# Kernel tuning notes

Hardware: AMD Instinct MI355X
Metric: run time of the kernel (lower is better)

Reference implementation:

```python
import jax, jax.numpy as jnp
import numpy as np

DEPTH, DIM, HEADS, DHEAD, MLP, CTX_DIM = 4, 1024, 16, 64, 4096, 1024
INNER = HEADS * DHEAD
SCALE = DHEAD ** -0.5
B, N, M = 4, 1024, 2048


def setup_inputs() -> dict:
    key = jax.random.key(0)
    ks = jax.random.split(key, 16)
    w = lambda k, shape: jax.random.normal(k, shape, dtype=jnp.float32) * 0.02
    return {
        "x": jax.random.normal(ks[0], (B, N, DIM), dtype=jnp.float32),
        "context": jax.random.normal(ks[1], (B, M, CTX_DIM), dtype=jnp.float32),
        "mask": jnp.ones((B, N), dtype=jnp.int32),
        # LayerNorm params: index 0 = pre-self-attn, 1 = pre-cross-attn, 2 = pre-FFN
        "ln_g": jnp.ones((DEPTH, 3, DIM), dtype=jnp.float32),
        "ln_b": jnp.zeros((DEPTH, 3, DIM), dtype=jnp.float32),
        "Wqkv": w(ks[2], (DEPTH, DIM, 3 * INNER)),
        "Wo_sa": w(ks[3], (DEPTH, INNER, DIM)),
        "bo_sa": jnp.zeros((DEPTH, DIM), dtype=jnp.float32),
        "Wkv": w(ks[4], (DEPTH, CTX_DIM, 2 * INNER)),
        "Wq": w(ks[5], (DEPTH, DIM, INNER)),
        "Wo_ca": w(ks[6], (DEPTH, INNER, DIM)),
        "bo_ca": jnp.zeros((DEPTH, DIM), dtype=jnp.float32),
        "W1": w(ks[7], (DEPTH, DIM, MLP)),
        "b1": jnp.zeros((DEPTH, MLP), dtype=jnp.float32),
        "W2": w(ks[8], (DEPTH, MLP, DIM)),
        "b2": jnp.zeros((DEPTH, DIM), dtype=jnp.float32),
    }


def _ln(x, g, b, eps=1e-5):
    mu = jnp.mean(x, axis=-1, keepdims=True)
    var = jnp.var(x, axis=-1, keepdims=True)
    return (x - mu) * jax.lax.rsqrt(var + eps) * g + b


def _split_heads(t):  # [b, n, h*d] -> [b, h, n, d]
    b, n, _ = t.shape
    return t.reshape(b, n, HEADS, DHEAD).transpose(0, 2, 1, 3)


def _merge_heads(t):  # [b, h, n, d] -> [b, n, h*d]
    b, h, n, d = t.shape
    return t.transpose(0, 2, 1, 3).reshape(b, n, h * d)


def _forward(x, context, mask, ln_g, ln_b, Wqkv, Wo_sa, bo_sa, Wkv, Wq, Wo_ca, bo_ca, W1, b1, W2, b2):
    neg_mask = (1 - mask).astype(x.dtype)  # [b, n]
    for i in range(DEPTH):
        # ---- self-attention (PreNorm) ----
        h = _ln(x, ln_g[i, 0], ln_b[i, 0])
        qkv = h @ Wqkv[i]
        q, k, v = jnp.split(qkv, 3, axis=-1)
        q, k, v = _split_heads(q), _split_heads(k), _split_heads(v)
        dots = jnp.einsum('bhnd,bhmd->bhnm', q, k) * SCALE
        dots = dots - neg_mask[:, None, None, :] * 1e11  # mask over keys
        attn = jax.nn.softmax(dots, axis=-1)
        out = _merge_heads(jnp.einsum('bhnm,bhmd->bhnd', attn, v))
        x = x + out @ Wo_sa[i] + bo_sa[i]
        # ---- cross-attention (PreNorm) ----
        h = _ln(x, ln_g[i, 1], ln_b[i, 1])
        kv = context @ Wkv[i]
        k, v = jnp.split(kv, 2, axis=-1)
        q = _split_heads(h @ Wq[i])
        k, v = _split_heads(k), _split_heads(v)
        dots = jnp.einsum('bhnd,bhmd->bhnm', q, k) * SCALE  # [b, h, n, m]
        dots = dots - neg_mask[:, None, :, None] * 1e6  # mask over queries
        attn = jax.nn.softmax(dots, axis=-1)
        out = _merge_heads(jnp.einsum('bhnm,bhmd->bhnd', attn, v))
        x = x + out @ Wo_ca[i] + bo_ca[i]
        # ---- feed-forward (PreNorm) ----
        h = _ln(x, ln_g[i, 2], ln_b[i, 2])
        h = jax.nn.gelu(h @ W1[i] + b1[i], approximate=False)
        x = x + h @ W2[i] + b2[i]
    return x


def reference(x, context, mask, ln_g, ln_b, Wqkv, Wo_sa, bo_sa, Wkv, Wq, Wo_ca, bo_ca, W1, b1, W2, b2):
    return _forward(x, context, mask, ln_g, ln_b, Wqkv, Wo_sa, bo_sa, Wkv, Wq, Wo_ca, bo_ca, W1, b1, W2, b2)
```

## Files before the change

kernel.cpp:

```cpp
#include <hip/hip_runtime.h>
#include <math.h>

#define DEPTH_ 4
#define DIM_ 1024
#define HEADS_ 16
#define DHEAD_ 64
#define MLP_ 4096
#define CTX_ 1024
#define INNER_ 1024
#define B_ 4
#define N_ 1024
#define M_ 2048

typedef unsigned short u16;
typedef __attribute__((ext_vector_type(4))) unsigned short u16x4;
typedef __attribute__((ext_vector_type(8))) short bf16x8;
typedef __attribute__((ext_vector_type(4))) float f32x4;
typedef __attribute__((ext_vector_type(4))) int i32x4;

#define SCQ 0.18033688011112042f

__device__ __forceinline__ u16 f2bf(float f) {
    unsigned u = __float_as_uint(f);
    return (u16)((u + 0x7fffu + ((u >> 16) & 1u)) >> 16);
}

__device__ __forceinline__ float bf2f(u16 v) {
    return __uint_as_float(((unsigned)v) << 16);
}

__device__ __forceinline__ float exp2_fast(float x) {
    float r;
    asm("v_exp_f32 %0, %1" : "=v"(r) : "v"(x));
    return r;
}

__device__ __forceinline__ float rcp_fast(float x) {
    float r;
    asm("v_rcp_f32 %0, %1" : "=v"(r) : "v"(x));
    return r;
}

__device__ __forceinline__ unsigned cvt_pk_bf16(float lo, float hi) {
    unsigned r;
    asm("v_cvt_pk_bf16_f32 %0, %1, %2" : "=v"(r) : "v"(lo), "v"(hi));
    return r;
}

__device__ __forceinline__ float gelu_fast(float v) {
    float t = v + 0.044715f * v * v * v;
    float e = exp2_fast(-2.302221673f * t);
    return v * rcp_fast(1.0f + e);
}

#define GLOAD16(gp, sp)                                                        \
    __builtin_amdgcn_global_load_lds(                                          \
        (const __attribute__((address_space(1))) void*)(gp),                   \
        (__attribute__((address_space(3))) void*)(sp), 16, 0, 0)

template <int MODE>
__global__ __launch_bounds__(256) void ln_res(
    float* __restrict__ x, const u16* __restrict__ d0,
    const u16* __restrict__ d1, const float* __restrict__ dbias,
    const float* __restrict__ g, const float* __restrict__ b,
    u16* __restrict__ y) {
    int row = blockIdx.x;
    float4 v = ((const float4*)(x + (size_t)row * DIM_))[threadIdx.x];
    if constexpr (MODE == 1) {
        u16x4 a0 = ((const u16x4*)(d0 + (size_t)row * DIM_))[threadIdx.x];
        u16x4 a1 = ((const u16x4*)(d1 + (size_t)row * DIM_))[threadIdx.x];
        float4 bb4 = ((const float4*)dbias)[threadIdx.x];
        v.x += bf2f(a0[0]) + bf2f(a1[0]) + bb4.x;
        v.y += bf2f(a0[1]) + bf2f(a1[1]) + bb4.y;
        v.z += bf2f(a0[2]) + bf2f(a1[2]) + bb4.z;
        v.w += bf2f(a0[3]) + bf2f(a1[3]) + bb4.w;
        ((float4*)(x + (size_t)row * DIM_))[threadIdx.x] = v;
    }
    float s  = v.x + v.y + v.z + v.w;
    float ss = v.x * v.x + v.y * v.y + v.z * v.z + v.w * v.w;
    #pragma unroll
    for (int off = 32; off; off >>= 1) {
        s  += __shfl_down(s, off);
        ss += __shfl_down(ss, off);
    }
    __shared__ float red[10];
    int wid = threadIdx.x >> 6, lane = threadIdx.x & 63;
    if (lane == 0) { red[wid] = s; red[4 + wid] = ss; }
    __syncthreads();
    if (threadIdx.x == 0) {
        float ts  = red[0] + red[1] + red[2] + red[3];
        float tss = red[4] + red[5] + red[6] + red[7];
        float mu  = ts * (1.0f / DIM_);
        float var = tss * (1.0f / DIM_) - mu * mu;
        red[8] = mu;
        red[9] = rsqrtf(var + 1e-5f);
    }
    __syncthreads();
    float mu = red[8], rs = red[9];
    float4 gg = ((const float4*)g)[threadIdx.x];
    float4 bb = ((const float4*)b)[threadIdx.x];
    u16x4 o;
    o[0] = f2bf((v.x - mu) * rs * gg.x + bb.x);
    o[1] = f2bf((v.y - mu) * rs * gg.y + bb.y);
    o[2] = f2bf((v.z - mu) * rs * gg.z + bb.z);
    o[3] = f2bf((v.w - mu) * rs * gg.w + bb.w);
    ((u16x4*)(y + (size_t)row * DIM_))[threadIdx.x] = o;
}

__global__ __launch_bounds__(256) void res_add(
    float* __restrict__ x, const u16* __restrict__ d0,
    const u16* __restrict__ d1, const float* __restrict__ dbias) {
    int row = blockIdx.x;
    float4 v = ((const float4*)(x + (size_t)row * DIM_))[threadIdx.x];
    u16x4 a0 = ((const u16x4*)(d0 + (size_t)row * DIM_))[threadIdx.x];
    u16x4 a1 = ((const u16x4*)(d1 + (size_t)row * DIM_))[threadIdx.x];
    float4 bb4 = ((const float4*)dbias)[threadIdx.x];
    v.x += bf2f(a0[0]) + bf2f(a1[0]) + bb4.x;
    v.y += bf2f(a0[1]) + bf2f(a1[1]) + bb4.y;
    v.z += bf2f(a0[2]) + bf2f(a1[2]) + bb4.z;
    v.w += bf2f(a0[3]) + bf2f(a1[3]) + bb4.w;
    ((float4*)(x + (size_t)row * DIM_))[threadIdx.x] = v;
}

__global__ __launch_bounds__(256) void cast_kernel(const float* __restrict__ in,
                                                   u16* __restrict__ out) {
    int i = blockIdx.x * 256 + threadIdx.x;
    float4 v = ((const float4*)in)[i];
    u16x4 o = {f2bf(v.x), f2bf(v.y), f2bf(v.z), f2bf(v.w)};
    ((u16x4*)out)[i] = o;
}

struct PrepArgs {
    const float* src[7];
    int K[7];
    int N[7];
    int dstOff[7];
    int tileCum[7];
};

__global__ __launch_bounds__(256) void prep_weights(PrepArgs a,
                                                    u16* __restrict__ wt) {
    __shared__ float tile[32][33];
    int bid = blockIdx.x;
    int wi = 0;
    while (bid >= a.tileCum[wi]) ++wi;
    int tbase = wi ? a.tileCum[wi - 1] : 0;
    int tid = bid - tbase;
    int Kd = a.K[wi], Nd = a.N[wi];
    int ntx = Nd >> 5;
    int bx = (tid % ntx) * 32;
    int by = (tid / ntx) * 32;
    const float* W = a.src[wi];
    u16* Wt = wt + a.dstOff[wi];

    int t = threadIdx.x;
    int kl = t >> 3, n4 = (t & 7) * 4;
    float4 v = *(const float4*)(W + (size_t)(by + kl) * Nd + bx + n4);
    tile[kl][n4 + 0] = v.x; tile[kl][n4 + 1] = v.y;
    tile[kl][n4 + 2] = v.z; tile[kl][n4 + 3] = v.w;
    __syncthreads();
    int nl = t >> 3, k4 = (t & 7) * 4;
    u16x4 o;
    #pragma unroll
    for (int j = 0; j < 4; ++j) o[j] = f2bf(tile[k4 + j][nl]);
    *(u16x4*)(Wt + (size_t)(bx + nl) * Kd + by + k4) = o;
}

template <int EPI, int SPLITK>
__global__ __launch_bounds__(256, 3) void gemm_mfma3(
    const u16* __restrict__ A, const u16* __restrict__ Bt,
    const float* __restrict__ bias, void* __restrict__ Cout,
    u16* __restrict__ vt, int Mdim, int Ndim, int Kdim, int nx, int ny) {
    __shared__ __align__(16) u16 As[3][128 * 32];
    __shared__ __align__(16) u16 Bs[3][128 * 32];
    const int t = threadIdx.x;
    const int lane = t & 63, w = t >> 6;
    const int c = lane & 15, g = lane >> 4;
    const int wy = w >> 1, wx = w & 1;

    const int nwg = gridDim.x;
    const int wid = (blockIdx.x & 7) * (nwg >> 3) + (blockIdx.x >> 3);
    const int bx = wid % nx;
    const int by = (wid / nx) % ny;
    const int bz = wid / (nx * ny);
    const int m0 = by * 128, n0 = bx * 128;

    f32x4 acc[4][4] = {};

    const int srow = w * 32 + (lane >> 2);
    const int scb  = (((lane & 3) ^ ((srow >> 1) & 3)) * 8);
    const u16* Ag = A + (size_t)(m0 + srow) * Kdim + scb;
    const u16* Bg = Bt + (size_t)(n0 + srow) * Kdim + scb;

    auto stage = [&](int buf, int k0) {
        GLOAD16(Ag + k0, &As[buf][w * 1024]);
        GLOAD16(Ag + k0 + (size_t)16 * Kdim, &As[buf][w * 1024 + 512]);
        GLOAD16(Bg + k0, &Bs[buf][w * 1024]);
        GLOAD16(Bg + k0 + (size_t)16 * Kdim, &Bs[buf][w * 1024 + 512]);
    };
    const int rsw = (c >> 1) & 3;
    auto compute = [&](int buf) {
        bf16x8 a[4], b[4];
        #pragma unroll
        for (int i = 0; i < 4; ++i)
            a[i] = *(const bf16x8*)&As[buf][(wy * 64 + i * 16 + c) * 32 +
                                            ((g ^ rsw) * 8)];
        #pragma unroll
        for (int j = 0; j < 4; ++j)
            b[j] = *(const bf16x8*)&Bs[buf][(wx * 64 + j * 16 + c) * 32 +
                                            ((g ^ rsw) * 8)];
        __builtin_amdgcn_s_setprio(1);
        #pragma unroll
        for (int i = 0; i < 4; ++i)
            #pragma unroll
            for (int j = 0; j < 4; ++j)
                acc[i][j] = __builtin_amdgcn_mfma_f32_16x16x32_bf16(
                    a[i], b[j], acc[i][j], 0, 0, 0);
        __builtin_amdgcn_s_setprio(0);
    };

    const int kchunk = Kdim / SPLITK;
    const int kbeg = bz * kchunk;
    const int nsteps = kchunk / 32;

    stage(0, kbeg);
    stage(1, kbeg + 32);
    int cb = 0, sb = 2;
    for (int s = 0; s < nsteps; ++s) {
        if (s + 1 < nsteps)
            asm volatile("s_waitcnt vmcnt(4)" ::: "memory");
        else
            asm volatile("s_waitcnt vmcnt(0)" ::: "memory");
        __builtin_amdgcn_s_barrier();
        if (s + 2 < nsteps) {
            stage(sb, kbeg + (s + 2) * 32);
            sb = (sb == 2) ? 0 : sb + 1;
        }
        compute(cb);
        cb = (cb == 2) ? 0 : cb + 1;
    }

    constexpr int VTHRESH = (EPI == 4) ? 2048 : 1024;
    constexpr int RPB     = (EPI == 4) ? 1024 : 2048;
    constexpr int KVL     = (EPI == 4) ? 1024 : 2048;

    const size_t outOff = (SPLITK > 1) ? (size_t)bz * Mdim * Ndim : 0;

    #pragma unroll
    for (int i = 0; i < 4; ++i) {
        int row0 = m0 + wy * 64 + i * 16 + g * 4;
        #pragma unroll
        for (int j = 0; j < 4; ++j) {
            int col = n0 + wx * 64 + j * 16 + c;
            u16x4 o4;
            #pragma unroll
            for (int r = 0; r < 4; ++r) {
                float v = acc[i][j][r];
                size_t idx = (size_t)(row0 + r) * Ndim + col;
                if constexpr (EPI == 0) {
                    ((u16*)Cout)[outOff + idx] = f2bf(v);
                } else if constexpr (EPI == 4) {
                    if (col < 1024) v *= SCQ;
                    u16 bv = f2bf(v);
                    ((u16*)Cout)[idx] = bv;
                    o4[r] = bv;
                } else if constexpr (EPI == 5) {
                    u16 bv = f2bf(v);
                    ((u16*)Cout)[idx] = bv;
                    o4[r] = bv;
                } else if constexpr (EPI == 6) {
                    ((u16*)Cout)[idx] = f2bf(v * SCQ);
                } else if constexpr (EPI == 1) {
                    v += bias[col];
                    ((u16*)Cout)[idx] = f2bf(gelu_fast(v));
                }
            }
            if constexpr (EPI == 4 || EPI == 5) {
                if (n0 + wx * 64 + j * 16 >= VTHRESH) {
                    int hh = (col - VTHRESH) >> 6;
                    int dd = col & 63;
                    int bi = row0 / RPB;
                    int kv = row0 % RPB;
                    *(u16x4*)&vt[(((size_t)bi * HEADS_ + hh) * 64 + dd) * KVL +
                                 kv] = o4;
                }
            }
        }
    }
}

template <int KLEN, int IS_SA>
__global__ __launch_bounds__(256) void attn_mfma2(
    const u16* __restrict__ Qsrc, const u16* __restrict__ Ksrc,
    const u16* __restrict__ Vtg, const int* __restrict__ mask,
    u16* __restrict__ O) {
    constexpr int QSTR = IS_SA ? 3 * INNER_ : INNER_;
    constexpr int KSTR = IS_SA ? 3 * INNER_ : 2 * INNER_;
    constexpr int KOFF = IS_SA ? INNER_ : 0;

    __shared__ __align__(16) u16 Ks[2][64 * 64];
    __shared__ __align__(16) u16 Vs[2][64 * 64];

    const int t = threadIdx.x;
    const int lane = t & 63, w = t >> 6;
    const int c = lane & 15, g = lane >> 4;

    const int nwg = gridDim.x;
    const int wid = (blockIdx.x & 7) * (nwg >> 3) + (blockIdx.x >> 3);
    const int qb = wid & 15;
    const int h  = (wid >> 4) & 15;
    const int bb = wid >> 8;
    const int q0 = qb * 64;
    const int kvbase = bb * KLEN;

    const u16* qp =
        Qsrc + (size_t)(bb * N_ + q0 + w * 16 + c) * QSTR + h * 64 + g * 8;
    bf16x8 qf[2];
    qf[0] = *(const bf16x8*)qp;
    qf[1] = *(const bf16x8*)(qp + 32);

    const int sl_r = lane >> 3;
    const int scol = ((lane & 7) ^ sl_r) * 8;
    const int r0 = w * 16, r1 = w * 16 + 8;
    const u16* Kg0 = Ksrc + (size_t)(kvbase + r0 + sl_r) * KSTR + KOFF +
                     h * 64 + scol;
    const u16* Kg1 = Ksrc + (size_t)(kvbase + r1 + sl_r) * KSTR + KOFF +
                     h * 64 + scol;
    const u16* Vg0 =
        Vtg + ((size_t)(bb * HEADS_ + h) * 64 + r0 + sl_r) * KLEN + scol;
    const u16* Vg1 =
        Vtg + ((size_t)(bb * HEADS_ + h) * 64 + r1 + sl_r) * KLEN + scol;

    auto stageKV = [&](int buf, int kt) {
        GLOAD16(Kg0 + (size_t)kt * 64 * KSTR, &Ks[buf][r0 * 64]);
        GLOAD16(Kg1 + (size_t)kt * 64 * KSTR, &Ks[buf][r1 * 64]);
        GLOAD16(Vg0 + kt * 64, &Vs[buf][r0 * 64]);
        GLOAD16(Vg1 + kt * 64, &Vs[buf][r1 * 64]);
    };

    f32x4 o[4] = {};
    float mr = -1e30f, lr = 0.f;
    const int srcA = c + 32 * (g & 1);
    const int srcB = srcA + 16;
    const bool hi = (g & 2) != 0;
    constexpr int NT = KLEN / 64;

    stageKV(0, 0);
    __syncthreads();
    int cur = 0;

    for (int kt = 0; kt < NT; ++kt) {
        if (kt + 1 < NT) stageKV(cur ^ 1, kt + 1);

        f32x4 sv[4] = {};
        #pragma unroll
        for (int kvb = 0; kvb < 4; ++kvb) {
            #pragma unroll
            for (int f = 0; f < 2; ++f) {
                bf16x8 kf = *(const bf16x8*)&Ks[cur][(kvb * 16 + c) * 64 +
                                                     (((g + 4 * f) ^ (c & 7)) * 8)];
                sv[kvb] = __builtin_amdgcn_mfma_f32_16x16x32_bf16(
                    kf, qf[f], sv[kvb], 0, 0, 0);
            }
        }

        if constexpr (IS_SA) {
            int mbit = mask[bb * N_ + kt * 64 + lane];
            unsigned long long ball = __ballot(mbit != 0);
            if (ball != ~0ull) {
                float negm_reg = mbit ? 0.f : 2.0e10f;
                #pragma unroll
                for (int kvb = 0; kvb < 4; ++kvb)
                    #pragma unroll
                    for (int r = 0; r < 4; ++r)
                        sv[kvb][r] -= __shfl(negm_reg, kvb * 16 + g * 4 + r);
            }
        }

        float tm = sv[0][0];
        #pragma unroll
        for (int kvb = 0; kvb < 4; ++kvb)
            #pragma unroll
            for (int r = 0; r < 4; ++r) tm = fmaxf(tm, sv[kvb][r]);
        tm = fmaxf(tm, __shfl_xor(tm, 16));
        tm = fmaxf(tm, __shfl_xor(tm, 32));

        if (!__all(tm - mr <= 8.0f)) {
            float mn = fmaxf(mr, tm);
            float corr = exp2_fast(mr - mn);
            mr = mn;
            lr *= corr;
            float corrO[4];
            #pragma unroll
            for (int r = 0; r < 4; ++r) corrO[r] = __shfl(corr, g * 4 + r);
            #pragma unroll
            for (int db = 0; db < 4; ++db)
                #pragma unroll
                for (int r = 0; r < 4; ++r) o[db][r] *= corrO[r];
        }

        float ps = 0.f;
        #pragma unroll
        for (int kvb = 0; kvb < 4; ++kvb)
            #pragma unroll
            for (int r = 0; r < 4; ++r) {
                float p = exp2_fast(sv[kvb][r] - mr);
                sv[kvb][r] = p;
                ps += p;
            }
        ps += __shfl_xor(ps, 16);
        ps += __shfl_xor(ps, 32);
        lr += ps;

        unsigned pk[4][2];
        #pragma unroll
        for (int kvb = 0; kvb < 4; ++kvb)
            #pragma unroll
            for (int j = 0; j < 2; ++j)
                pk[kvb][j] = cvt_pk_bf16(sv[kvb][2 * j], sv[kvb][2 * j + 1]);

        #pragma unroll
        for (int pv = 0; pv < 2; ++pv) {
            int a0 = __shfl((int)pk[2 * pv][0], srcA);
            int b0 = __shfl((int)pk[2 * pv + 1][0], srcA);
            int a1 = __shfl((int)pk[2 * pv][1], srcA);
            int b1 = __shfl((int)pk[2 * pv + 1][1], srcA);
            int a2 = __shfl((int)pk[2 * pv][0], srcB);
            int b2 = __shfl((int)pk[2 * pv + 1][0], srcB);
            int a3 = __shfl((int)pk[2 * pv][1], srcB);
            int b3 = __shfl((int)pk[2 * pv + 1][1], srcB);
            i32x4 tw = {hi ? b0 : a0, hi ? b1 : a1, hi ? b2 : a2,
                        hi ? b3 : a3};
            bf16x8 pa = *(bf16x8*)&tw;
            #pragma unroll
            for (int db = 0; db < 4; ++db) {
                bf16x8 vf = *(const bf16x8*)&Vs[cur][(db * 16 + c) * 64 +
                                                     (((g + 4 * pv) ^ (c & 7)) * 8)];
                o[db] = __builtin_amdgcn_mfma_f32_16x16x32_bf16(pa, vf, o[db],
                                                                0, 0, 0);
            }
        }
        __syncthreads();
        cur ^= 1;
    }

    float inv = rcp_fast(lr);
    float invO[4];
    #pragma unroll
    for (int r = 0; r < 4; ++r) invO[r] = __shfl(inv, g * 4 + r);
    #pragma unroll
    for (int db = 0; db < 4; ++db)
        #pragma unroll
        for (int r = 0; r < 4; ++r) {
            size_t idx =
                (size_t)(bb * N_ + q0 + w * 16 + g * 4 + r) * INNER_ +
                h * 64 + db * 16 + c;
            O[idx] = f2bf(o[db][r] * invO[r]);
        }
}

extern "C" void kernel_launch(void* const* d_in, const int* in_sizes, int n_in,
                              void* d_out, int out_size, void* d_ws,
                              size_t ws_size, hipStream_t stream) {
    const float* x     = (const float*)d_in[0];
    const float* ctx   = (const float*)d_in[1];
    const int*   mask  = (const int*)d_in[2];
    const float* ln_g  = (const float*)d_in[3];
    const float* ln_b  = (const float*)d_in[4];
    const float* Wqkv  = (const float*)d_in[5];
    const float* Wo_sa = (const float*)d_in[6];
    const float* bo_sa = (const float*)d_in[7];
    const float* Wkv   = (const float*)d_in[8];
    const float* Wq    = (const float*)d_in[9];
    const float* Wo_ca = (const float*)d_in[10];
    const float* bo_ca = (const float*)d_in[11];
    const float* W1    = (const float*)d_in[12];
    const float* b1    = (const float*)d_in[13];
    const float* W2    = (const float*)d_in[14];
    const float* b2    = (const float*)d_in[15];
    float* xout = (float*)d_out;

    char* ws = (char*)d_ws;
    u16* lnout = (u16*)ws;
    u16* big   = (u16*)(ws + (8ull << 20));
    u16* qca   = (u16*)(ws + (40ull << 20));
    u16* ctxb  = (u16*)(ws + (48ull << 20));
    u16* wt    = (u16*)(ws + (64ull << 20));
    u16* vt_sa = (u16*)(ws + (96ull << 20));
    u16* R1    = (u16*)(ws + (104ull << 20));
    u16* aout  = lnout;

    const int O_QKV = 0;
    const int O_WOSA = 3145728;
    const int O_WQ   = 4194304;
    const int O_WKV  = 5242880;
    const int O_WOCA = 7340032;
    const int O_W1   = 8388608;
    const int O_W2   = 12582912;

    hipMemcpyAsync(xout, x, sizeof(float) * B_ * N_ * DIM_,
                   hipMemcpyDeviceToDevice, stream);
    cast_kernel<<<B_ * M_ * CTX_ / 1024, 256, 0, stream>>>(ctx, ctxb);

    const int ROWS = B_ * N_;
    const int CROWS = B_ * M_;
    const int HALF = ROWS * DIM_;
    dim3 blk(256);

    for (int i = 0; i < DEPTH_; ++i) {
        const float* g  = ln_g + (size_t)(i * 3) * DIM_;
        const float* bb = ln_b + (size_t)(i * 3) * DIM_;

        PrepArgs pa;
        pa.src[0] = Wqkv  + (size_t)i * DIM_ * 3 * INNER_;
        pa.src[1] = Wo_sa + (size_t)i * INNER_ * DIM_;
        pa.src[2] = Wq    + (size_t)i * DIM_ * INNER_;
        pa.src[3] = Wkv   + (size_t)i * CTX_ * 2 * INNER_;
        pa.src[4] = Wo_ca + (size_t)i * INNER_ * DIM_;
        pa.src[5] = W1    + (size_t)i * DIM_ * MLP_;
        pa.src[6] = W2    + (size_t)i * MLP_ * DIM_;
        int Ks_[7] = {1024, 1024, 1024, 1024, 1024, 1024, 4096};
        int Ns_[7] = {3072, 1024, 1024, 2048, 1024, 4096, 1024};
        int Of_[7] = {O_QKV, O_WOSA, O_WQ, O_WKV, O_WOCA, O_W1, O_W2};
        int cum = 0;
        for (int k = 0; k < 7; ++k) {
            pa.K[k] = Ks_[k]; pa.N[k] = Ns_[k]; pa.dstOff[k] = Of_[k];
            cum += (Ks_[k] / 32) * (Ns_[k] / 32);
            pa.tileCum[k] = cum;
        }
        prep_weights<<<cum, blk, 0, stream>>>(pa, wt);

        if (i == 0)
            ln_res<0><<<ROWS, blk, 0, stream>>>(xout, nullptr, nullptr,
                                                nullptr, g, bb, lnout);
        else
            ln_res<1><<<ROWS, blk, 0, stream>>>(xout, R1, R1 + HALF,
                                                b2 + (size_t)(i - 1) * DIM_,
                                                g, bb, lnout);
        gemm_mfma3<4, 1><<<24 * 32, blk, 0, stream>>>(
            lnout, wt + O_QKV, nullptr, big, vt_sa, ROWS, 3 * INNER_, DIM_,
            24, 32);
        attn_mfma2<N_, 1><<<1024, blk, 0, stream>>>(big, big, vt_sa, mask,
                                                    aout);
        gemm_mfma3<0, 2><<<8 * 32 * 2, blk, 0, stream>>>(
            aout, wt + O_WOSA, nullptr, R1, nullptr, ROWS, DIM_, INNER_,
            8, 32);

        ln_res<1><<<ROWS, blk, 0, stream>>>(xout, R1, R1 + HALF,
                                            bo_sa + (size_t)i * DIM_,
                                            g + DIM_, bb + DIM_, lnout);
        gemm_mfma3<6, 1><<<8 * 32, blk, 0, stream>>>(
            lnout, wt + O_WQ, nullptr, qca, nullptr, ROWS, INNER_, DIM_,
            8, 32);
        gemm_mfma3<5, 1><<<16 * 64, blk, 0, stream>>>(
            ctxb, wt + O_WKV, nullptr, big, R1, CROWS, 2 * INNER_, CTX_,
            16, 64);
        attn_mfma2<M_, 0><<<1024, blk, 0, stream>>>(qca, big, R1, mask,
                                                    aout);
        gemm_mfma3<0, 2><<<8 * 32 * 2, blk, 0, stream>>>(
            aout, wt + O_WOCA, nullptr, R1, nullptr, ROWS, DIM_, INNER_,
            8, 32);

        ln_res<1><<<ROWS, blk, 0, stream>>>(xout, R1, R1 + HALF,
                                            bo_ca + (size_t)i * DIM_,
                                            g + 2 * DIM_, bb + 2 * DIM_,
                                            lnout);
        gemm_mfma3<1, 1><<<32 * 32, blk, 0, stream>>>(
            lnout, wt + O_W1, b1 + (size_t)i * MLP_, big, nullptr, ROWS, MLP_,
            DIM_, 32, 32);
        gemm_mfma3<0, 2><<<8 * 32 * 2, blk, 0, stream>>>(
            big, wt + O_W2, nullptr, R1, nullptr, ROWS, DIM_, MLP_, 8, 32);
    }
    res_add<<<ROWS, blk, 0, stream>>>(xout, R1, R1 + HALF,
                                      b2 + (size_t)(DEPTH_ - 1) * DIM_);
}
```

Baseline: 1.713 ms.

## Permute V-transpose layout so P feeds PV MFMA without cross-lane shuffles

The V-transpose written by the projection epilogue now uses a permuted key ordering (kv_sigma). That ordering lets the packed softmax probabilities be fed directly as the A operand of the PV MFMA, removing eight shuffles and selects per half-tile. The running row-sum is now kept per lane across the loop and reduced once at the end, and the row-max shuffle reduction runs only when a rescale is needed. This cuts cross-lane traffic in the attention inner loop. In exchange it adds accumulator registers and a coupled layout contract between the projection GEMM and the attention kernel.

```diff
diff --git a/kernel.cpp b/kernel.cpp
--- a/kernel.cpp
+++ b/kernel.cpp
@@ -51,6 +51,11 @@
     float t = v + 0.044715f * v * v * v;
     float e = exp2_fast(-2.302221673f * t);
     return v * rcp_fast(1.0f + e);
+}
+
+__device__ __forceinline__ int kv_sigma(int kv) {
+    return (kv & ~31) | (((kv >> 2) & 3) << 3) | (((kv >> 4) & 1) << 2) |
+           (kv & 3);
 }
 
 #define GLOAD16(gp, sp)                                                        \
@@ -281,8 +286,9 @@
                     int dd = col & 63;
                     int bi = row0 / RPB;
                     int kv = row0 % RPB;
+                    int kvs = kv_sigma(kv);
                     *(u16x4*)&vt[(((size_t)bi * HEADS_ + hh) * 64 + dd) * KVL +
-                                 kv] = o4;
+                                 kvs] = o4;
                 }
             }
         }
@@ -339,10 +345,8 @@
     };
 
     f32x4 o[4] = {};
-    float mr = -1e30f, lr = 0.f;
-    const int srcA = c + 32 * (g & 1);
-    const int srcB = srcA + 16;
-    const bool hi = (g & 2) != 0;
+    f32x4 lracc[4] = {};
+    float mr = -1e30f;
     constexpr int NT = KLEN / 64;
 
     stageKV(0, 0);
@@ -382,14 +386,17 @@
         for (int kvb = 0; kvb < 4; ++kvb)
             #pragma unroll
             for (int r = 0; r < 4; ++r) tm = fmaxf(tm, sv[kvb][r]);
-        tm = fmaxf(tm, __shfl_xor(tm, 16));
-        tm = fmaxf(tm, __shfl_xor(tm, 32));
 
         if (!__all(tm - mr <= 8.0f)) {
-            float mn = fmaxf(mr, tm);
+            float tmc = fmaxf(tm, __shfl_xor(tm, 16));
+            tmc = fmaxf(tmc, __shfl_xor(tmc, 32));
+            float mn = fmaxf(mr, tmc);
             float corr = exp2_fast(mr - mn);
             mr = mn;
-            lr *= corr;
+            #pragma unroll
+            for (int kvb = 0; kvb < 4; ++kvb)
+                #pragma unroll
+                for (int r = 0; r < 4; ++r) lracc[kvb][r] *= corr;
             float corrO[4];
             #pragma unroll
             for (int r = 0; r < 4; ++r) corrO[r] = __shfl(corr, g * 4 + r);
@@ -399,18 +406,14 @@
                 for (int r = 0; r < 4; ++r) o[db][r] *= corrO[r];
         }
 
-        float ps = 0.f;
         #pragma unroll
         for (int kvb = 0; kvb < 4; ++kvb)
             #pragma unroll
             for (int r = 0; r < 4; ++r) {
                 float p = exp2_fast(sv[kvb][r] - mr);
                 sv[kvb][r] = p;
-                ps += p;
+                lracc[kvb][r] += p;
             }
-        ps += __shfl_xor(ps, 16);
-        ps += __shfl_xor(ps, 32);
-        lr += ps;
 
         unsigned pk[4][2];
         #pragma unroll
@@ -421,16 +424,8 @@
 
         #pragma unroll
         for (int pv = 0; pv < 2; ++pv) {
-            int a0 = __shfl((int)pk[2 * pv][0], srcA);
-            int b0 = __shfl((int)pk[2 * pv + 1][0], srcA);
-            int a1 = __shfl((int)pk[2 * pv][1], srcA);
-            int b1 = __shfl((int)pk[2 * pv + 1][1], srcA);
-            int a2 = __shfl((int)pk[2 * pv][0], srcB);
-            int b2 = __shfl((int)pk[2 * pv + 1][0], srcB);
-            int a3 = __shfl((int)pk[2 * pv][1], srcB);
-            int b3 = __shfl((int)pk[2 * pv + 1][1], srcB);
-            i32x4 tw = {hi ? b0 : a0, hi ? b1 : a1, hi ? b2 : a2,
-                        hi ? b3 : a3};
+            i32x4 tw = {(int)pk[2 * pv][0], (int)pk[2 * pv][1],
+                        (int)pk[2 * pv + 1][0], (int)pk[2 * pv + 1][1]};
             bf16x8 pa = *(bf16x8*)&tw;
             #pragma unroll
             for (int db = 0; db < 4; ++db) {
@@ -443,6 +438,14 @@
         __syncthreads();
         cur ^= 1;
     }
+
+    float lr = 0.f;
+    #pragma unroll
+    for (int kvb = 0; kvb < 4; ++kvb)
+        #pragma unroll
+        for (int r = 0; r < 4; ++r) lr += lracc[kvb][r];
+    lr += __shfl_xor(lr, 16);
+    lr += __shfl_xor(lr, 32);
 
     float inv = rcp_fast(lr);
     float invO[4];
```

New measurement: 1.625 ms. -5.2%, faster.
